# Kernel tuning notes

Hardware: AMD Instinct MI355X
Metric: run time of the kernel (lower is better)

Reference implementation:

```python
import jax, jax.numpy as jnp
import numpy as np

DENSITY_FACTOR = 100.0
RAY_SAMPLES = 256
W_RES, H_RES = 320, 240
BS = 4
VOL_D = 128


def setup_inputs() -> dict:
    key = jax.random.key(0)
    k1, k2 = jax.random.split(key)
    vol = jax.random.uniform(k1, (BS, 4, VOL_D, VOL_D, VOL_D), dtype=jnp.float32)
    # per-batch rigid rotation about the y axis (homogeneous 4x4, w component stays 1)
    ang = jax.random.uniform(k2, (BS,), minval=0.0, maxval=2.0 * np.pi, dtype=jnp.float32)
    c, s = jnp.cos(ang), jnp.sin(ang)
    z, o = jnp.zeros_like(c), jnp.ones_like(c)
    tfm = jnp.stack([
        jnp.stack([c, z, s, z], -1),
        jnp.stack([z, o, z, z], -1),
        jnp.stack([-s, z, c, z], -1),
        jnp.stack([z, z, z, o], -1),
    ], axis=1)  # (BS,4,4)
    return {"vol": vol, "tfm": tfm}


def grid_sample_3d(vol, grid):
    """torch.nn.functional.grid_sample (5D, trilinear, zeros padding, align_corners=False).
    vol: (C,D,H,W); grid: (S,Hh,Ww,3) with last dim = (x,y,z) in [-1,1]. -> (C,S,Hh,Ww)"""
    C, D, H, W = vol.shape
    gx, gy, gz = grid[..., 0], grid[..., 1], grid[..., 2]
    # unnormalize, align_corners=False convention
    ix = ((gx + 1.0) * W - 1.0) * 0.5
    iy = ((gy + 1.0) * H - 1.0) * 0.5
    iz = ((gz + 1.0) * D - 1.0) * 0.5
    ix0, iy0, iz0 = jnp.floor(ix), jnp.floor(iy), jnp.floor(iz)
    fx, fy, fz = ix - ix0, iy - iy0, iz - iz0
    out = jnp.zeros((C,) + grid.shape[:-1], vol.dtype)
    for dz in (0, 1):
        for dy in (0, 1):
            for dx in (0, 1):
                xi, yi, zi = ix0 + dx, iy0 + dy, iz0 + dz
                w = ((fx if dx else 1.0 - fx) * (fy if dy else 1.0 - fy)
                     * (fz if dz else 1.0 - fz))
                valid = ((xi >= 0) & (xi < W) & (yi >= 0) & (yi < H)
                         & (zi >= 0) & (zi < D))
                xc = jnp.clip(xi, 0, W - 1).astype(jnp.int32)
                yc = jnp.clip(yi, 0, H - 1).astype(jnp.int32)
                zc = jnp.clip(zi, 0, D - 1).astype(jnp.int32)
                v = vol[:, zc, yc, xc]  # (C,S,Hh,Ww) gather
                out = out + v * (w * valid.astype(vol.dtype))[None]
    return out


def _sample_coords(tfm):
    """Build the transformed sample grid: (BS, S, H, W, 3)."""
    z = jnp.linspace(-1.0, 1.0, RAY_SAMPLES)
    y = jnp.linspace(-1.0, 1.0, H_RES)
    x = jnp.linspace(-1.0, 1.0, W_RES)
    Z, Y, X = jnp.meshgrid(z, y, x, indexing='ij')  # torch.meshgrid default 'ij'
    coords = jnp.stack([X, Y, Z, jnp.ones_like(X)], axis=-1)  # (S,H,W,4) homogenized
    flat = coords.reshape(-1, 4)
    tc = jnp.einsum('bij,nj->bni', tfm, flat).reshape(
        tfm.shape[0], RAY_SAMPLES, H_RES, W_RES, 4)
    return tc[..., :3] / tc[..., 3:4]


def reference(vol, tfm):
    density = vol[:, 3:4]            # (B,1,D,H,W)
    color = vol[:, :3]               # (B,3,D,H,W)
    grid = _sample_coords(tfm.astype(vol.dtype))  # (B,S,H,W,3)
    dens = density * (DENSITY_FACTOR / RAY_SAMPLES)
    ds = jax.vmap(grid_sample_3d)(dens, grid)        # (B,1,S,H,W)
    transmission = jnp.cumprod(1.0 - ds, axis=2)     # sequential scan over rays
    weight = ds * transmission                       # (B,1,S,H,W)
    w_sum = jnp.sum(weight, axis=2)                  # (B,1,H,W)
    cs = jax.vmap(grid_sample_3d)(color, grid)       # (B,3,S,H,W)
    render = jnp.sum(weight * cs, axis=2) / (w_sum + 1e-6)  # (B,3,H,W)
    alpha = 1.0 - transmission[:, :, -1]             # == 1 - prod(1-ds, axis=2)
    return render * alpha
```

## Files before the change

### kernel.cpp

```cpp
#include <hip/hip_runtime.h>
#include <hip/hip_fp16.h>

namespace {

constexpr int W_RES = 320, H_RES = 240, BS = 4, VD = 128, NS = 256;
constexpr float DENS_SCALE = 100.0f / 256.0f;
constexpr float TAU = 5e-4f;
constexpr long long VOX = (long long)VD * VD * VD;

__device__ __forceinline__ unsigned h2u(__half2 h) {
    unsigned u; __builtin_memcpy(&u, &h, 4); return u;
}
__device__ __forceinline__ __half2 u2h(unsigned u) {
    __half2 h; __builtin_memcpy(&h, &u, 4); return h;
}

__global__ void transpose_k(const float* __restrict__ vol, uint4* __restrict__ out) {
    long long tid = (long long)blockIdx.x * blockDim.x + threadIdx.x;
    const long long npair = (long long)BS * VOX / 2;
    if (tid >= npair) return;
    int b = (int)(tid / (VOX / 2));
    long long r2 = (tid - (long long)b * (VOX / 2)) * 2;
    const float* vb = vol + (long long)b * 4 * VOX + r2;
    float2 R = *(const float2*)(vb);
    float2 G = *(const float2*)(vb + VOX);
    float2 Bc = *(const float2*)(vb + 2 * VOX);
    float2 Dn = *(const float2*)(vb + 3 * VOX);
    uint4 o;
    o.x = h2u(__floats2half2_rn(R.x, G.x));
    o.y = h2u(__floats2half2_rn(Bc.x, Dn.x));
    o.z = h2u(__floats2half2_rn(R.y, G.y));
    o.w = h2u(__floats2half2_rn(Bc.y, Dn.y));
    out[tid] = o;
}

struct Stage {
    uint2 p[8];
    float w[8];
};

struct Coord {
    int x0, y0, z0;
    float fx, fy, fz;
    bool fast;
};

__device__ __forceinline__ Coord make_coord(float ix, float iy, float iz) {
    Coord c;
    float fx0 = floorf(ix), fy0 = floorf(iy), fz0 = floorf(iz);
    c.fx = ix - fx0; c.fy = iy - fy0; c.fz = iz - fz0;
    c.x0 = (int)fx0; c.y0 = (int)fy0; c.z0 = (int)fz0;
    c.fast = ((unsigned)c.x0 < 127u) & ((unsigned)c.y0 < 127u) & ((unsigned)c.z0 < 127u);
    return c;
}

__device__ __forceinline__ void weights_plain(const Coord& c, Stage& st) {
    float wx0 = 1.0f - c.fx, wx1 = c.fx;
    float wy0 = 1.0f - c.fy, wy1 = c.fy;
    float wz0 = 1.0f - c.fz, wz1 = c.fz;
    float w00 = wz0 * wy0, w01 = wz0 * wy1, w10 = wz1 * wy0, w11 = wz1 * wy1;
    st.w[0] = w00 * wx0; st.w[1] = w00 * wx1;
    st.w[2] = w01 * wx0; st.w[3] = w01 * wx1;
    st.w[4] = w10 * wx0; st.w[5] = w10 * wx1;
    st.w[6] = w11 * wx0; st.w[7] = w11 * wx1;
}

__device__ __forceinline__ void stage_fast(const uint2* __restrict__ vb,
                                           const Coord& c, Stage& st) {
    const uint2* r0 = vb + ((c.z0 * VD + c.y0) * VD + c.x0);
    const uint2* r1 = r0 + VD * VD;
    st.p[0] = r0[0];      st.p[1] = r0[1];
    st.p[2] = r0[VD];     st.p[3] = r0[VD + 1];
    st.p[4] = r1[0];      st.p[5] = r1[1];
    st.p[6] = r1[VD];     st.p[7] = r1[VD + 1];
    weights_plain(c, st);
}

__device__ __forceinline__ void stage_safe(const uint2* __restrict__ vb,
                                           const Coord& c, Stage& st) {
    int x0 = c.x0, y0 = c.y0, z0 = c.z0;
    float mx0 = ((unsigned)x0 < 128u) ? 1.0f : 0.0f;
    float mx1 = ((unsigned)(x0 + 1) < 128u) ? 1.0f : 0.0f;
    float my0 = ((unsigned)y0 < 128u) ? 1.0f : 0.0f;
    float my1 = ((unsigned)(y0 + 1) < 128u) ? 1.0f : 0.0f;
    float mz0 = ((unsigned)z0 < 128u) ? 1.0f : 0.0f;
    float mz1 = ((unsigned)(z0 + 1) < 128u) ? 1.0f : 0.0f;
    float wx0 = (1.0f - c.fx) * mx0, wx1 = c.fx * mx1;
    float wy0 = (1.0f - c.fy) * my0, wy1 = c.fy * my1;
    float wz0 = (1.0f - c.fz) * mz0, wz1 = c.fz * mz1;

    int xc0 = min(max(x0, 0), 127), xc1 = min(max(x0 + 1, 0), 127);
    int yc0 = min(max(y0, 0), 127), yc1 = min(max(y0 + 1, 0), 127);
    int zc0 = min(max(z0, 0), 127), zc1 = min(max(z0 + 1, 0), 127);

    int r00 = (zc0 * VD + yc0) * VD, r01 = (zc0 * VD + yc1) * VD;
    int r10 = (zc1 * VD + yc0) * VD, r11 = (zc1 * VD + yc1) * VD;

    st.p[0] = vb[r00 + xc0]; st.p[1] = vb[r00 + xc1];
    st.p[2] = vb[r01 + xc0]; st.p[3] = vb[r01 + xc1];
    st.p[4] = vb[r10 + xc0]; st.p[5] = vb[r10 + xc1];
    st.p[6] = vb[r11 + xc0]; st.p[7] = vb[r11 + xc1];

    float w00 = wz0 * wy0, w01 = wz0 * wy1, w10 = wz1 * wy0, w11 = wz1 * wy1;
    st.w[0] = w00 * wx0; st.w[1] = w00 * wx1;
    st.w[2] = w01 * wx0; st.w[3] = w01 * wx1;
    st.w[4] = w10 * wx0; st.w[5] = w10 * wx1;
    st.w[6] = w11 * wx0; st.w[7] = w11 * wx1;
}

__device__ __forceinline__ void consume(const Stage& st, float& T, float& wsum,
                                        float& aR, float& aG, float& aB) {
    float ax0 = 0, ay0 = 0, az0 = 0, aw0 = 0;
    float ax1 = 0, ay1 = 0, az1 = 0, aw1 = 0;
#pragma unroll
    for (int i = 0; i < 8; i += 2) {
        __half2 rg0 = u2h(st.p[i].x), bd0 = u2h(st.p[i].y);
        __half2 rg1 = u2h(st.p[i + 1].x), bd1 = u2h(st.p[i + 1].y);
        ax0 = fmaf(st.w[i], __half2float(__low2half(rg0)), ax0);
        ay0 = fmaf(st.w[i], __half2float(__high2half(rg0)), ay0);
        az0 = fmaf(st.w[i], __half2float(__low2half(bd0)), az0);
        aw0 = fmaf(st.w[i], __half2float(__high2half(bd0)), aw0);
        ax1 = fmaf(st.w[i + 1], __half2float(__low2half(rg1)), ax1);
        ay1 = fmaf(st.w[i + 1], __half2float(__high2half(rg1)), ay1);
        az1 = fmaf(st.w[i + 1], __half2float(__low2half(bd1)), az1);
        aw1 = fmaf(st.w[i + 1], __half2float(__high2half(bd1)), aw1);
    }
    float dsv = (aw0 + aw1) * DENS_SCALE;
    T *= (1.0f - dsv);
    float wgt = dsv * T;
    wsum += wgt;
    aR = fmaf(wgt, ax0 + ax1, aR);
    aG = fmaf(wgt, ay0 + ay1, aG);
    aB = fmaf(wgt, az0 + az1, aB);
}

__global__ void __launch_bounds__(256) raycast_k(const uint2* __restrict__ vol8,
                                                 const float* __restrict__ tfm,
                                                 float* __restrict__ out) {
    constexpr int NPIX = W_RES * H_RES;
    int lane = threadIdx.x & 63;
    int wave = threadIdx.x >> 6;
    int bx = blockIdx.x % (W_RES / 16);
    int rest = blockIdx.x / (W_RES / 16);
    int by = rest % (H_RES / 16);
    int b = rest / (H_RES / 16);
    int x = bx * 16 + (lane & 15);
    int y = by * 16 + wave * 4 + (lane >> 4);

    float X = -1.0f + 2.0f * x / (float)(W_RES - 1);
    float Y = -1.0f + 2.0f * y / (float)(H_RES - 1);
    const float dZ = 2.0f / (float)(NS - 1);

    const float* M = tfm + b * 16;
    float bxc = M[0] * X + M[1] * Y + M[3];
    float byc = M[4] * X + M[5] * Y + M[7];
    float bzc = M[8] * X + M[9] * Y + M[11];
    float bwc = M[12] * X + M[13] * Y + M[15];
    float m02 = M[2], m12 = M[6], m22 = M[10], m32 = M[14];

    const uint2* vb = vol8 + (long long)b * VOX;

    bool w1 = (fabsf(bwc - 1.0f) < 1e-6f) && (fabsf(m32) < 1e-6f);
    float lo = 0.0f, hi = (float)(NS - 1);
    if (w1) {
        const float LIM = 1.0078125f + 1e-5f;
        auto clipAxis = [&](float bb, float mm) {
            float A = bb - mm;
            float B = mm * dZ;
            if (fabsf(B) < 1e-9f) {
                if (fabsf(A) > LIM) { lo = 1.0f; hi = 0.0f; }
            } else {
                float s1 = (-LIM - A) / B, s2 = (LIM - A) / B;
                lo = fmaxf(lo, fminf(s1, s2));
                hi = fminf(hi, fmaxf(s1, s2));
            }
        };
        clipAxis(bxc, m02);
        clipAxis(byc, m12);
        clipAxis(bzc, m22);
    }
    int s_start = max(0, (int)ceilf(lo - 1e-3f));
    int s_end = min(NS - 1, (int)floorf(hi + 1e-3f));

    int wsv = s_start, wev = s_end;
#pragma unroll
    for (int off = 1; off < 64; off <<= 1) {
        wsv = min(wsv, __shfl_xor(wsv, off));
        wev = max(wev, __shfl_xor(wev, off));
    }

    auto coords = [&](int s, float& ix, float& iy, float& iz) {
        float Z = fmaf((float)s, dZ, -1.0f);
        float gx = fmaf(m02, Z, bxc);
        float gy = fmaf(m12, Z, byc);
        float gz = fmaf(m22, Z, bzc);
        if (!w1) {
            float iw = 1.0f / fmaf(m32, Z, bwc);
            gx *= iw; gy *= iw; gz *= iw;
        }
        ix = fmaf(gx, 64.0f, 63.5f);
        iy = fmaf(gy, 64.0f, 63.5f);
        iz = fmaf(gz, 64.0f, 63.5f);
    };

    float T = 1.0f, wsum = 0.0f, aR = 0.0f, aG = 0.0f, aB = 0.0f;
    Stage A, B, C;

    for (int s = wsv; s <= wev; s += 3) {
        bool alive = (T >= TAU);
        bool g0 = (s >= s_start) & (s <= s_end) & alive;
        bool g1 = (s + 1 >= s_start) & (s + 1 <= s_end) & alive;
        bool g2 = (s + 2 >= s_start) & (s + 2 <= s_end) & alive;
        Coord c0, c1, c2;
        float ix, iy, iz;
        if (g0) { coords(s, ix, iy, iz); c0 = make_coord(ix, iy, iz); }
        if (g1) { coords(s + 1, ix, iy, iz); c1 = make_coord(ix, iy, iz); }
        if (g2) { coords(s + 2, ix, iy, iz); c2 = make_coord(ix, iy, iz); }
        bool fastAll = __all((g0 ? c0.fast : true) & (g1 ? c1.fast : true) &
                             (g2 ? c2.fast : true));
        if (fastAll) {
            if (g0) stage_fast(vb, c0, A);
            if (g1) stage_fast(vb, c1, B);
            if (g2) stage_fast(vb, c2, C);
        } else {
            if (g0) stage_safe(vb, c0, A);
            if (g1) stage_safe(vb, c1, B);
            if (g2) stage_safe(vb, c2, C);
        }
        __builtin_amdgcn_sched_barrier(0);
        if (g0) consume(A, T, wsum, aR, aG, aB);
        if (g1 & (T >= TAU)) consume(B, T, wsum, aR, aG, aB);
        if (g2 & (T >= TAU)) consume(C, T, wsum, aR, aG, aB);
        if (!__any((T >= TAU) & (s + 3 <= s_end))) break;
    }

    float scale = (1.0f - T) / (wsum + 1e-6f);
    int po = y * W_RES + x;
    float* ob = out + (long long)b * 3 * NPIX;
    ob[po] = aR * scale;
    ob[po + NPIX] = aG * scale;
    ob[po + 2 * NPIX] = aB * scale;
}

}

extern "C" void kernel_launch(void* const* d_in, const int* in_sizes, int n_in,
                              void* d_out, int out_size, void* d_ws, size_t ws_size,
                              hipStream_t stream) {
    const float* vol = (const float*)d_in[0];
    const float* tfm = (const float*)d_in[1];
    float* out = (float*)d_out;

    uint4* v16 = (uint4*)d_ws;
    (void)ws_size; (void)in_sizes; (void)n_in; (void)out_size;

    const long long npair = (long long)BS * VOX / 2;
    transpose_k<<<(int)((npair + 255) / 256), 256, 0, stream>>>(vol, v16);

    const int nblk = (W_RES / 16) * (H_RES / 16) * BS;
    raycast_k<<<nblk, 256, 0, stream>>>((const uint2*)v16, tfm, out);
}
```

Baseline: 173.0 us.

## Quantize volume to 8-bit RGBA with x-neighbor pairs packed per texel

Replaces the fp16 RGBA volume with 8-bit unorm channels. Each 8-byte element now holds a voxel together with its +x neighbor, so a trilinear sample needs four 8-byte loads instead of eight. Decoding uses integer shifts and converts, with the 1/255 factor folded into the density scale and the final output scale. This cuts gather traffic and cache footprint, but 8-bit quantization of uniform inputs brings error of about 1/510 per channel, which can amplify through the density cumprod and may break tolerance.

```diff
diff --git a/kernel.cpp b/kernel.cpp
--- a/kernel.cpp
+++ b/kernel.cpp
@@ -1,42 +1,49 @@
 #include <hip/hip_runtime.h>
-#include <hip/hip_fp16.h>
 
 namespace {
 
 constexpr int W_RES = 320, H_RES = 240, BS = 4, VD = 128, NS = 256;
-constexpr float DENS_SCALE = 100.0f / 256.0f;
+constexpr float DENS_SCALE = 100.0f / 256.0f / 255.0f;
 constexpr float TAU = 5e-4f;
 constexpr long long VOX = (long long)VD * VD * VD;
-
-__device__ __forceinline__ unsigned h2u(__half2 h) {
-    unsigned u; __builtin_memcpy(&u, &h, 4); return u;
-}
-__device__ __forceinline__ __half2 u2h(unsigned u) {
-    __half2 h; __builtin_memcpy(&h, &u, 4); return h;
-}
 
 __global__ void transpose_k(const float* __restrict__ vol, uint4* __restrict__ out) {
     long long tid = (long long)blockIdx.x * blockDim.x + threadIdx.x;
     const long long npair = (long long)BS * VOX / 2;
     if (tid >= npair) return;
     int b = (int)(tid / (VOX / 2));
-    long long r2 = (tid - (long long)b * (VOX / 2)) * 2;
-    const float* vb = vol + (long long)b * 4 * VOX + r2;
+    long long r = (tid - (long long)b * (VOX / 2)) * 2;
+    int x = (int)(r & (VD - 1));
+    bool last = (x == VD - 2);
+    const float* vb = vol + (long long)b * 4 * VOX + r;
     float2 R = *(const float2*)(vb);
     float2 G = *(const float2*)(vb + VOX);
-    float2 Bc = *(const float2*)(vb + 2 * VOX);
+    float2 Bl = *(const float2*)(vb + 2 * VOX);
     float2 Dn = *(const float2*)(vb + 3 * VOX);
+    float R2 = last ? 0.0f : vb[2];
+    float G2 = last ? 0.0f : vb[VOX + 2];
+    float B2 = last ? 0.0f : vb[2 * VOX + 2];
+    float D2 = last ? 0.0f : vb[3 * VOX + 2];
+    auto pk = [](float r_, float g_, float bl_, float d_) -> unsigned {
+        unsigned ur = (unsigned)(r_ * 255.0f + 0.5f);
+        unsigned ug = (unsigned)(g_ * 255.0f + 0.5f);
+        unsigned ub = (unsigned)(bl_ * 255.0f + 0.5f);
+        unsigned ud = (unsigned)(d_ * 255.0f + 0.5f);
+        return ur | (ug << 8) | (ub << 16) | (ud << 24);
+    };
+    unsigned p0 = pk(R.x, G.x, Bl.x, Dn.x);
+    unsigned p1 = pk(R.y, G.y, Bl.y, Dn.y);
+    unsigned p2 = pk(R2, G2, B2, D2);
     uint4 o;
-    o.x = h2u(__floats2half2_rn(R.x, G.x));
-    o.y = h2u(__floats2half2_rn(Bc.x, Dn.x));
-    o.z = h2u(__floats2half2_rn(R.y, G.y));
-    o.w = h2u(__floats2half2_rn(Bc.y, Dn.y));
+    o.x = p0; o.y = p1;
+    o.z = p1; o.w = p2;
     out[tid] = o;
 }
 
-struct Stage {
-    uint2 p[8];
-    float w[8];
+struct St {
+    uint2 p[4];
+    float wzy[4];
+    float wlo, whi;
 };
 
 struct Coord {
@@ -45,96 +52,86 @@
     bool fast;
 };
 
-__device__ __forceinline__ Coord make_coord(float ix, float iy, float iz) {
+__device__ __forceinline__ Coord mkc(float ix, float iy, float iz) {
     Coord c;
-    float fx0 = floorf(ix), fy0 = floorf(iy), fz0 = floorf(iz);
-    c.fx = ix - fx0; c.fy = iy - fy0; c.fz = iz - fz0;
-    c.x0 = (int)fx0; c.y0 = (int)fy0; c.z0 = (int)fz0;
-    c.fast = ((unsigned)c.x0 < 127u) & ((unsigned)c.y0 < 127u) & ((unsigned)c.z0 < 127u);
+    float f;
+    f = floorf(ix); c.fx = ix - f; c.x0 = (int)f;
+    f = floorf(iy); c.fy = iy - f; c.y0 = (int)f;
+    f = floorf(iz); c.fz = iz - f; c.z0 = (int)f;
+    c.fast = ((unsigned)c.x0 < 128u) & ((unsigned)c.y0 < 127u) & ((unsigned)c.z0 < 127u);
     return c;
 }
 
-__device__ __forceinline__ void weights_plain(const Coord& c, Stage& st) {
-    float wx0 = 1.0f - c.fx, wx1 = c.fx;
+__device__ __forceinline__ void stage_fast(const uint2* __restrict__ vb,
+                                           const Coord& c, St& st) {
+    const uint2* r0 = vb + ((c.z0 * VD + c.y0) * VD + c.x0);
+    const uint2* r1 = r0 + VD * VD;
+    st.p[0] = r0[0];
+    st.p[1] = r0[VD];
+    st.p[2] = r1[0];
+    st.p[3] = r1[VD];
+    st.wlo = 1.0f - c.fx;
+    st.whi = c.fx;
     float wy0 = 1.0f - c.fy, wy1 = c.fy;
     float wz0 = 1.0f - c.fz, wz1 = c.fz;
-    float w00 = wz0 * wy0, w01 = wz0 * wy1, w10 = wz1 * wy0, w11 = wz1 * wy1;
-    st.w[0] = w00 * wx0; st.w[1] = w00 * wx1;
-    st.w[2] = w01 * wx0; st.w[3] = w01 * wx1;
-    st.w[4] = w10 * wx0; st.w[5] = w10 * wx1;
-    st.w[6] = w11 * wx0; st.w[7] = w11 * wx1;
-}
-
-__device__ __forceinline__ void stage_fast(const uint2* __restrict__ vb,
-                                           const Coord& c, Stage& st) {
-    const uint2* r0 = vb + ((c.z0 * VD + c.y0) * VD + c.x0);
-    const uint2* r1 = r0 + VD * VD;
-    st.p[0] = r0[0];      st.p[1] = r0[1];
-    st.p[2] = r0[VD];     st.p[3] = r0[VD + 1];
-    st.p[4] = r1[0];      st.p[5] = r1[1];
-    st.p[6] = r1[VD];     st.p[7] = r1[VD + 1];
-    weights_plain(c, st);
+    st.wzy[0] = wz0 * wy0; st.wzy[1] = wz0 * wy1;
+    st.wzy[2] = wz1 * wy0; st.wzy[3] = wz1 * wy1;
 }
 
 __device__ __forceinline__ void stage_safe(const uint2* __restrict__ vb,
-                                           const Coord& c, Stage& st) {
+                                           const Coord& c, St& st) {
     int x0 = c.x0, y0 = c.y0, z0 = c.z0;
-    float mx0 = ((unsigned)x0 < 128u) ? 1.0f : 0.0f;
-    float mx1 = ((unsigned)(x0 + 1) < 128u) ? 1.0f : 0.0f;
+    bool in01x = ((unsigned)x0 < 128u);
+    bool ism1 = (x0 == -1);
+    st.wlo = in01x ? (1.0f - c.fx) : (ism1 ? c.fx : 0.0f);
+    st.whi = in01x ? c.fx : 0.0f;
+    int bx = min(max(x0, 0), 127);
+
     float my0 = ((unsigned)y0 < 128u) ? 1.0f : 0.0f;
     float my1 = ((unsigned)(y0 + 1) < 128u) ? 1.0f : 0.0f;
     float mz0 = ((unsigned)z0 < 128u) ? 1.0f : 0.0f;
     float mz1 = ((unsigned)(z0 + 1) < 128u) ? 1.0f : 0.0f;
-    float wx0 = (1.0f - c.fx) * mx0, wx1 = c.fx * mx1;
+    int yc0 = min(max(y0, 0), 127), yc1 = min(max(y0 + 1, 0), 127);
+    int zc0 = min(max(z0, 0), 127), zc1 = min(max(z0 + 1, 0), 127);
+
+    st.p[0] = vb[(zc0 * VD + yc0) * VD + bx];
+    st.p[1] = vb[(zc0 * VD + yc1) * VD + bx];
+    st.p[2] = vb[(zc1 * VD + yc0) * VD + bx];
+    st.p[3] = vb[(zc1 * VD + yc1) * VD + bx];
+
     float wy0 = (1.0f - c.fy) * my0, wy1 = c.fy * my1;
     float wz0 = (1.0f - c.fz) * mz0, wz1 = c.fz * mz1;
-
-    int xc0 = min(max(x0, 0), 127), xc1 = min(max(x0 + 1, 0), 127);
-    int yc0 = min(max(y0, 0), 127), yc1 = min(max(y0 + 1, 0), 127);
-    int zc0 = min(max(z0, 0), 127), zc1 = min(max(z0 + 1, 0), 127);
-
-    int r00 = (zc0 * VD + yc0) * VD, r01 = (zc0 * VD + yc1) * VD;
-    int r10 = (zc1 * VD + yc0) * VD, r11 = (zc1 * VD + yc1) * VD;
-
-    st.p[0] = vb[r00 + xc0]; st.p[1] = vb[r00 + xc1];
-    st.p[2] = vb[r01 + xc0]; st.p[3] = vb[r01 + xc1];
-    st.p[4] = vb[r10 + xc0]; st.p[5] = vb[r10 + xc1];
-    st.p[6] = vb[r11 + xc0]; st.p[7] = vb[r11 + xc1];
-
-    float w00 = wz0 * wy0, w01 = wz0 * wy1, w10 = wz1 * wy0, w11 = wz1 * wy1;
-    st.w[0] = w00 * wx0; st.w[1] = w00 * wx1;
-    st.w[2] = w01 * wx0; st.w[3] = w01 * wx1;
-    st.w[4] = w10 * wx0; st.w[5] = w10 * wx1;
-    st.w[6] = w11 * wx0; st.w[7] = w11 * wx1;
-}
-
-__device__ __forceinline__ void consume(const Stage& st, float& T, float& wsum,
+    st.wzy[0] = wz0 * wy0; st.wzy[1] = wz0 * wy1;
+    st.wzy[2] = wz1 * wy0; st.wzy[3] = wz1 * wy1;
+}
+
+__device__ __forceinline__ void consume(const St& st, float& T, float& wsum,
                                         float& aR, float& aG, float& aB) {
-    float ax0 = 0, ay0 = 0, az0 = 0, aw0 = 0;
-    float ax1 = 0, ay1 = 0, az1 = 0, aw1 = 0;
+    float ar = 0, ag = 0, ab = 0, ad = 0;
 #pragma unroll
-    for (int i = 0; i < 8; i += 2) {
-        __half2 rg0 = u2h(st.p[i].x), bd0 = u2h(st.p[i].y);
-        __half2 rg1 = u2h(st.p[i + 1].x), bd1 = u2h(st.p[i + 1].y);
-        ax0 = fmaf(st.w[i], __half2float(__low2half(rg0)), ax0);
-        ay0 = fmaf(st.w[i], __half2float(__high2half(rg0)), ay0);
-        az0 = fmaf(st.w[i], __half2float(__low2half(bd0)), az0);
-        aw0 = fmaf(st.w[i], __half2float(__high2half(bd0)), aw0);
-        ax1 = fmaf(st.w[i + 1], __half2float(__low2half(rg1)), ax1);
-        ay1 = fmaf(st.w[i + 1], __half2float(__high2half(rg1)), ay1);
-        az1 = fmaf(st.w[i + 1], __half2float(__low2half(bd1)), az1);
-        aw1 = fmaf(st.w[i + 1], __half2float(__high2half(bd1)), aw1);
-    }
-    float dsv = (aw0 + aw1) * DENS_SCALE;
+    for (int i = 0; i < 4; ++i) {
+        unsigned lo = st.p[i].x, hi = st.p[i].y;
+        float wl = st.wzy[i] * st.wlo;
+        float wh = st.wzy[i] * st.whi;
+        ar = fmaf(wl, (float)(lo & 255u), ar);
+        ag = fmaf(wl, (float)((lo >> 8) & 255u), ag);
+        ab = fmaf(wl, (float)((lo >> 16) & 255u), ab);
+        ad = fmaf(wl, (float)(lo >> 24), ad);
+        ar = fmaf(wh, (float)(hi & 255u), ar);
+        ag = fmaf(wh, (float)((hi >> 8) & 255u), ag);
+        ab = fmaf(wh, (float)((hi >> 16) & 255u), ab);
+        ad = fmaf(wh, (float)(hi >> 24), ad);
+    }
+    float dsv = ad * DENS_SCALE;
     T *= (1.0f - dsv);
     float wgt = dsv * T;
     wsum += wgt;
-    aR = fmaf(wgt, ax0 + ax1, aR);
-    aG = fmaf(wgt, ay0 + ay1, aG);
-    aB = fmaf(wgt, az0 + az1, aB);
-}
-
-__global__ void __launch_bounds__(256) raycast_k(const uint2* __restrict__ vol8,
+    aR = fmaf(wgt, ar, aR);
+    aG = fmaf(wgt, ag, aG);
+    aB = fmaf(wgt, ab, aB);
+}
+
+__global__ void __launch_bounds__(256) raycast_k(const uint2* __restrict__ vol,
                                                  const float* __restrict__ tfm,
                                                  float* __restrict__ out) {
     constexpr int NPIX = W_RES * H_RES;
@@ -158,7 +155,7 @@
     float bwc = M[12] * X + M[13] * Y + M[15];
     float m02 = M[2], m12 = M[6], m22 = M[10], m32 = M[14];
 
-    const uint2* vb = vol8 + (long long)b * VOX;
+    const uint2* vb = vol + (long long)b * VOX;
 
     bool w1 = (fabsf(bwc - 1.0f) < 1e-6f) && (fabsf(m32) < 1e-6f);
     float lo = 0.0f, hi = (float)(NS - 1);
@@ -166,11 +163,11 @@
         const float LIM = 1.0078125f + 1e-5f;
         auto clipAxis = [&](float bb, float mm) {
             float A = bb - mm;
-            float B = mm * dZ;
-            if (fabsf(B) < 1e-9f) {
+            float Bq = mm * dZ;
+            if (fabsf(Bq) < 1e-9f) {
                 if (fabsf(A) > LIM) { lo = 1.0f; hi = 0.0f; }
             } else {
-                float s1 = (-LIM - A) / B, s2 = (LIM - A) / B;
+                float s1 = (-LIM - A) / Bq, s2 = (LIM - A) / Bq;
                 lo = fmaxf(lo, fminf(s1, s2));
                 hi = fminf(hi, fmaxf(s1, s2));
             }
@@ -204,7 +201,7 @@
     };
 
     float T = 1.0f, wsum = 0.0f, aR = 0.0f, aG = 0.0f, aB = 0.0f;
-    Stage A, B, C;
+    St S0, S1, S2;
 
     for (int s = wsv; s <= wev; s += 3) {
         bool alive = (T >= TAU);
@@ -213,28 +210,28 @@
         bool g2 = (s + 2 >= s_start) & (s + 2 <= s_end) & alive;
         Coord c0, c1, c2;
         float ix, iy, iz;
-        if (g0) { coords(s, ix, iy, iz); c0 = make_coord(ix, iy, iz); }
-        if (g1) { coords(s + 1, ix, iy, iz); c1 = make_coord(ix, iy, iz); }
-        if (g2) { coords(s + 2, ix, iy, iz); c2 = make_coord(ix, iy, iz); }
+        if (g0) { coords(s, ix, iy, iz); c0 = mkc(ix, iy, iz); }
+        if (g1) { coords(s + 1, ix, iy, iz); c1 = mkc(ix, iy, iz); }
+        if (g2) { coords(s + 2, ix, iy, iz); c2 = mkc(ix, iy, iz); }
         bool fastAll = __all((g0 ? c0.fast : true) & (g1 ? c1.fast : true) &
                              (g2 ? c2.fast : true));
         if (fastAll) {
-            if (g0) stage_fast(vb, c0, A);
-            if (g1) stage_fast(vb, c1, B);
-            if (g2) stage_fast(vb, c2, C);
+            if (g0) stage_fast(vb, c0, S0);
+            if (g1) stage_fast(vb, c1, S1);
+            if (g2) stage_fast(vb, c2, S2);
         } else {
-            if (g0) stage_safe(vb, c0, A);
-            if (g1) stage_safe(vb, c1, B);
-            if (g2) stage_safe(vb, c2, C);
+            if (g0) stage_safe(vb, c0, S0);
+            if (g1) stage_safe(vb, c1, S1);
+            if (g2) stage_safe(vb, c2, S2);
         }
         __builtin_amdgcn_sched_barrier(0);
-        if (g0) consume(A, T, wsum, aR, aG, aB);
-        if (g1 & (T >= TAU)) consume(B, T, wsum, aR, aG, aB);
-        if (g2 & (T >= TAU)) consume(C, T, wsum, aR, aG, aB);
+        if (g0) consume(S0, T, wsum, aR, aG, aB);
+        if (g1 & (T >= TAU)) consume(S1, T, wsum, aR, aG, aB);
+        if (g2 & (T >= TAU)) consume(S2, T, wsum, aR, aG, aB);
         if (!__any((T >= TAU) & (s + 3 <= s_end))) break;
     }
 
-    float scale = (1.0f - T) / (wsum + 1e-6f);
+    float scale = (1.0f - T) / (wsum + 1e-6f) * (1.0f / 255.0f);
     int po = y * W_RES + x;
     float* ob = out + (long long)b * 3 * NPIX;
     ob[po] = aR * scale;
@@ -251,12 +248,12 @@
     const float* tfm = (const float*)d_in[1];
     float* out = (float*)d_out;
 
-    uint4* v16 = (uint4*)d_ws;
+    uint4* v8 = (uint4*)d_ws;
     (void)ws_size; (void)in_sizes; (void)n_in; (void)out_size;
 
     const long long npair = (long long)BS * VOX / 2;
-    transpose_k<<<(int)((npair + 255) / 256), 256, 0, stream>>>(vol, v16);
+    transpose_k<<<(int)((npair + 255) / 256), 256, 0, stream>>>(vol, v8);
 
     const int nblk = (W_RES / 16) * (H_RES / 16) * BS;
-    raycast_k<<<nblk, 256, 0, stream>>>((const uint2*)v16, tfm, out);
-}
+    raycast_k<<<nblk, 256, 0, stream>>>((const uint2*)v8, tfm, out);
+}
```

New measurement: 148.5 us. 1.16x faster.
